# Optimization experiments

Hardware: AMD Instinct MI355X
Metric: run time of the kernel (lower is better)

Reference implementation:

```python
import jax, jax.numpy as jnp
import numpy as np

D_K = 64  # per-head dim, used as softmax scale (matches __init__ d_k)

def setup_inputs() -> dict:
    key = jax.random.key(0)
    kq, kk, kv, km = jax.random.split(key, 4)
    B, H, S, D = 2, 16, 2048, D_K
    q = jax.random.normal(kq, (B, H, S, D), dtype=jnp.float32)
    k = jax.random.normal(kk, (B, H, S, D), dtype=jnp.float32)
    v = jax.random.normal(kv, (B, H, S, D), dtype=jnp.float32)
    mask = jax.random.randint(km, (B, 1, S, S), 0, 2).astype(jnp.bool_)
    return {"q": q, "k": k, "v": v, "mask": mask}

def reference(q, k, v, mask):
    # attn = (q / sqrt(d_k)) @ k^T  -> [B,H,S,S]
    scale = 1.0 / jnp.sqrt(jnp.float32(D_K))
    attn = jnp.einsum("bhqd,bhkd->bhqk", q * scale, k)
    # faithful to torch masked_fill(mask, -1e-09) -- note tiny value, not -1e9
    attn = jnp.where(mask, jnp.float32(-1e-9), attn)
    weights = jax.nn.softmax(attn, axis=-1)  # dropout p=0.0 -> identity
    output = jnp.einsum("bhqk,bhkd->bhqd", weights, v)
    return (output, weights)
```

## Files before the change

### kernel.cpp

```cpp
#include <hip/hip_runtime.h>
#include <hip/hip_bf16.h>


namespace {

constexpr int kS = 2048;
constexpr int kD = 64;
constexpr int kBH = 32;
constexpr int kTQW = 16;
constexpr int kNW = 4;
constexpr int kTQB = kTQW * kNW;
constexpr int kChunk = 64;
constexpr int kNC = kS / kChunk;
constexpr int kNB = kBH * (kS / kTQB);
constexpr size_t kWOff = (size_t)kBH * kS * kD;

typedef __attribute__((ext_vector_type(8))) short bf16x8;
typedef __attribute__((ext_vector_type(4))) short bf16x4;
typedef __attribute__((ext_vector_type(4))) float f32x4;

__device__ inline short f2bf(float f) {
  union { float f; unsigned u; } x; x.f = f;
  return (short)((x.u + 0x7fffu + ((x.u >> 16) & 1u)) >> 16);
}

__device__ inline unsigned pk2bf(float a, float b) {
  return (unsigned)(unsigned short)f2bf(a) | ((unsigned)(unsigned short)f2bf(b) << 16);
}

__device__ inline bf16x8 cvt8(float4 a, float4 b, float scale) {
  bf16x8 f;
  f[0] = f2bf(a.x * scale); f[1] = f2bf(a.y * scale);
  f[2] = f2bf(a.z * scale); f[3] = f2bf(a.w * scale);
  f[4] = f2bf(b.x * scale); f[5] = f2bf(b.y * scale);
  f[6] = f2bf(b.z * scale); f[7] = f2bf(b.w * scale);
  return f;
}

__device__ inline f32x4 mfma32(bf16x8 a, bf16x8 b, f32x4 c) {
  return __builtin_amdgcn_mfma_f32_16x16x32_bf16(a, b, c, 0, 0, 0);
}

__device__ inline f32x4 mfma16(bf16x4 a, bf16x4 b, f32x4 c) {
#if __has_builtin(__builtin_amdgcn_mfma_f32_16x16x16bf16_1k)
  return __builtin_amdgcn_mfma_f32_16x16x16bf16_1k(a, b, c, 0, 0, 0);
#elif __has_builtin(__builtin_amdgcn_mfma_f32_16x16x16_bf16)
  return __builtin_amdgcn_mfma_f32_16x16x16_bf16(a, b, c, 0, 0, 0);
#else
  f32x4 d = c;
  asm volatile("v_mfma_f32_16x16x16_bf16 %0, %1, %2, %0" : "+v"(d) : "v"(a), "v"(b));
  return d;
#endif
}

__device__ inline void block_sync_lds() {
  asm volatile("s_waitcnt lgkmcnt(0)" ::: "memory");
  __builtin_amdgcn_s_barrier();
  asm volatile("" ::: "memory");
}

__global__ __launch_bounds__(256, 4) void attn_fused(
    const float* __restrict__ qg, const float* __restrict__ kg,
    const float* __restrict__ vg, const unsigned int* __restrict__ mg,
    float* __restrict__ outg) {
  __shared__ __align__(16) short SH[18432];
  short (*K0)[72] = (short(*)[72])(SH);
  short (*K1)[72] = (short(*)[72])(SH + 4608);
  short (*V0)[72] = (short(*)[72])(SH + 9216);
  short (*V1)[72] = (short(*)[72])(SH + 13824);

  const int tid  = threadIdx.x;
  const int wv   = tid >> 6;
  const int lane = tid & 63;
  const int l15  = lane & 15;
  const int quad = lane >> 4;

  const int bid  = blockIdx.x;
  const int work = ((bid & 7) << 7) | (bid >> 3);
  const int qt   = work & 31;
  const int bh   = work >> 5;
  const int b    = bh >> 4;
  const int q0b  = qt * kTQB;

  int allW32 = 1, allI32 = 1, allBF = 1;
#pragma unroll
  for (int i = 0; i < 64; ++i) {
    const unsigned u = mg[i];
    const unsigned lo = u & 0xFFFFu, hi = u >> 16;
    allW32 &= (int)(u == 0u || u == 0x3F800000u);
    allI32 &= (int)(u == 0u || u == 1u);
    allBF  &= (int)((lo == 0u || lo == 0x3F80u) && (hi == 0u || hi == 0x3F80u));
  }
  int msz;
  if (allI32)      msz = 4;
  else if (allW32) msz = 4;
  else if (allBF)  msz = 2;
  else             msz = 1;
  const unsigned char* mB = (const unsigned char*)mg + (size_t)b * kS * kS * msz;

  const float* qbase = qg + (size_t)bh * kS * kD;
  const float* kbase = kg + (size_t)bh * kS * kD;
  const float* vbase = vg + (size_t)bh * kS * kD;
  float* obase = outg + (size_t)bh * kS * kD;
  float* wbase = outg + kWOff + (size_t)bh * kS * kS;

  const int qrow = q0b + wv * kTQW + l15;

  bf16x8 aq[2];
#pragma unroll
  for (int dh = 0; dh < 2; ++dh) {
    const float* p = qbase + (size_t)qrow * kD + dh * 32 + quad * 8;
    aq[dh] = cvt8(*(const float4*)p, *(const float4*)(p + 4), 0.125f);
  }

  const int si = tid >> 2;
  const int sj = (tid & 3) << 4;
  const int vd = (tid & 7) << 3;
  const int vk = (tid >> 3) << 1;
  float4 rk[4], rv[4];

  auto k_issue = [&](int c) {
    const float* p = kbase + (size_t)(c * kChunk + si) * kD + sj;
    rk[0] = *(const float4*)p;       rk[1] = *(const float4*)(p + 4);
    rk[2] = *(const float4*)(p + 8); rk[3] = *(const float4*)(p + 12);
  };
  auto k_write = [&](short (*Kdst)[72]) {
    *(bf16x8*)&Kdst[si][sj]     = cvt8(rk[0], rk[1], 1.0f);
    *(bf16x8*)&Kdst[si][sj + 8] = cvt8(rk[2], rk[3], 1.0f);
  };

  auto v_issue = [&](int c) {
    const float* p = vbase + (size_t)(c * kChunk + vk) * kD + vd;
    rv[0] = *(const float4*)p;        rv[1] = *(const float4*)(p + 4);
    rv[2] = *(const float4*)(p + kD); rv[3] = *(const float4*)(p + kD + 4);
  };
  auto v_write = [&](short (*Vdst)[72]) {
    const float* lo = (const float*)&rv[0];
    const float* hi = (const float*)&rv[2];
#pragma unroll
    for (int d = 0; d < 8; ++d) {
      const int dd = vd + d;
      const int ps = (vk >> 1) ^ (((dd >> 3) & 7) << 2);
      *(unsigned*)&Vdst[dd][2 * ps] = pk2bf(lo[d], hi[d]);
    }
  };

  uint4 mr[4];
  unsigned mu[4];
  auto m_issue = [&](int c) {
    const int col0 = c * kChunk + quad * 4;
#pragma unroll
    for (int t = 0; t < 4; ++t) {
      const size_t e = (size_t)qrow * kS + col0 + t * 16;
      if (msz == 1)      mr[t].x = *(const unsigned*)(mB + e);
      else if (msz == 4) mr[t]   = *(const uint4*)((const unsigned*)mB + e);
      else {
        const unsigned* p = (const unsigned*)((const unsigned short*)mB + e);
        mr[t].x = p[0]; mr[t].y = p[1];
      }
    }
  };
  auto m_conv = [&]() {
#pragma unroll
    for (int t = 0; t < 4; ++t) {
      if (msz == 1)      mu[t] = mr[t].x;
      else if (msz == 4) mu[t] = (mr[t].x ? 1u : 0u) | ((mr[t].y ? 1u : 0u) << 8) |
                                 ((mr[t].z ? 1u : 0u) << 16) | ((mr[t].w ? 1u : 0u) << 24);
      else {
        const unsigned a = mr[t].x, bb = mr[t].y;
        mu[t] = ((a & 0xFFFFu) ? 1u : 0u) | (((a >> 16) ? 1u : 0u) << 8) |
                (((bb & 0xFFFFu) ? 1u : 0u) << 16) | (((bb >> 16) ? 1u : 0u) << 24);
      }
    }
  };

  float lsum = 0.f;
  k_issue(0); k_write(K0); k_issue(1);
  block_sync_lds();
  for (int c = 0; c < kNC; ++c) {
    m_issue(c);
    if (c + 1 < kNC) k_write((c & 1) ? K0 : K1);
    if (c + 2 < kNC) k_issue(c + 2);
    m_conv();
    short (*K)[72] = (c & 1) ? K1 : K0;
#pragma unroll
    for (int t = 0; t < 4; ++t) {
      bf16x8 f0 = *(const bf16x8*)&K[t * 16 + l15][quad * 8];
      bf16x8 f1 = *(const bf16x8*)&K[t * 16 + l15][32 + quad * 8];
      f32x4 acc = {0.f, 0.f, 0.f, 0.f};
      acc = mfma32(f0, aq[0], acc);
      acc = mfma32(f1, aq[1], acc);
#pragma unroll
      for (int r = 0; r < 4; ++r) {
        const float e = __expf(acc[r]);
        lsum += ((mu[t] >> (8 * r)) & 0xFFu) ? 1.0f : e;
      }
    }
    block_sync_lds();
  }

  lsum += __shfl_xor(lsum, 16);
  lsum += __shfl_xor(lsum, 32);
  const float inv = 1.0f / lsum;

  f32x4 acco[4];
#pragma unroll
  for (int d = 0; d < 4; ++d) acco[d] = (f32x4){0.f, 0.f, 0.f, 0.f};

  k_issue(0); v_issue(0);
  k_write(K0); v_write(V0);
  k_issue(1); v_issue(1);
  block_sync_lds();
  float* const wrow = wbase + (size_t)qrow * kS;
  for (int c = 0; c < kNC; ++c) {
    m_issue(c);
    if (c + 1 < kNC) { k_write((c & 1) ? K0 : K1); v_write((c & 1) ? V0 : V1); }
    if (c + 2 < kNC) { k_issue(c + 2); v_issue(c + 2); }
    m_conv();
    short (*K)[72] = (c & 1) ? K1 : K0;
    short (*V)[72] = (c & 1) ? V1 : V0;
    __builtin_amdgcn_s_setprio(1);
#pragma unroll
    for (int t = 0; t < 4; ++t) {
      bf16x8 f0 = *(const bf16x8*)&K[t * 16 + l15][quad * 8];
      bf16x8 f1 = *(const bf16x8*)&K[t * 16 + l15][32 + quad * 8];
      f32x4 acc = {0.f, 0.f, 0.f, 0.f};
      acc = mfma32(f0, aq[0], acc);
      acc = mfma32(f1, aq[1], acc);
      const unsigned m = mu[t];
      const float w0 = ((m       & 0xFFu) ? 1.0f : __expf(acc[0])) * inv;
      const float w1 = ((m >> 8  & 0xFFu) ? 1.0f : __expf(acc[1])) * inv;
      const float w2 = ((m >> 16 & 0xFFu) ? 1.0f : __expf(acc[2])) * inv;
      const float w3 = ((m >> 24        ) ? 1.0f : __expf(acc[3])) * inv;
      *(f32x4*)(wrow + c * kChunk + t * 16 + quad * 4) = (f32x4){w0, w1, w2, w3};
      const bf16x4 wfrag = {f2bf(w0), f2bf(w1), f2bf(w2), f2bf(w3)};
#pragma unroll
      for (int dt = 0; dt < 4; ++dt) {
        const int dd = dt * 16 + l15;
        const int pp = (8 * t + 2 * quad) ^ (((dd >> 3) & 7) << 2);
        const bf16x4 vfrag = *(const bf16x4*)&V[dd][2 * pp];
        acco[dt] = mfma16(vfrag, wfrag, acco[dt]);
      }
    }
    __builtin_amdgcn_s_setprio(0);
    block_sync_lds();
  }

#pragma unroll
  for (int dt = 0; dt < 4; ++dt)
    *(f32x4*)(obase + (size_t)qrow * kD + dt * 16 + quad * 4) = acco[dt];
}

}

extern "C" void kernel_launch(void* const* d_in, const int* in_sizes, int n_in,
                              void* d_out, int out_size, void* d_ws, size_t ws_size,
                              hipStream_t stream) {
  const float* q = (const float*)d_in[0];
  const float* k = (const float*)d_in[1];
  const float* v = (const float*)d_in[2];
  const unsigned int* mask = (const unsigned int*)d_in[3];
  float* out = (float*)d_out;
  attn_fused<<<dim3(kNB), dim3(256), 0, stream>>>(q, k, v, mask, out);
}
```

Measured before the change: 905.1 us.

## Stage mask tiles through LDS as bitmasks with coalesced prefetched loads

Mask loading moves from per-lane scattered global reads, issued and consumed within the same chunk, to coalesced cooperative loads of the block's 64x64 mask tile. Each tile is compressed to a 16-bit-per-thread bitmask and double-buffered in LDS two chunks ahead, like K/V. Lanes then read one 64-bit word from LDS per chunk. This removes exposed mask-load latency and uncoalesced access, at the cost of a little extra LDS and bit-packing ALU work. The first pass also gains s_setprio around its MFMA section.

Result: faster. 811.5 us (-10.3%).

```diff
diff --git a/kernel.cpp b/kernel.cpp
--- a/kernel.cpp
+++ b/kernel.cpp
@@ -63,11 +63,13 @@
     const float* __restrict__ qg, const float* __restrict__ kg,
     const float* __restrict__ vg, const unsigned int* __restrict__ mg,
     float* __restrict__ outg) {
-  __shared__ __align__(16) short SH[18432];
+  __shared__ __align__(16) short SH[18944];
   short (*K0)[72] = (short(*)[72])(SH);
   short (*K1)[72] = (short(*)[72])(SH + 4608);
   short (*V0)[72] = (short(*)[72])(SH + 9216);
   short (*V1)[72] = (short(*)[72])(SH + 13824);
+  unsigned short* Msk0 = (unsigned short*)(SH + 18432);
+  unsigned short* Msk1 = (unsigned short*)(SH + 18688);
 
   const int tid  = threadIdx.x;
   const int wv   = tid >> 6;
@@ -105,6 +107,7 @@
   float* wbase = outg + kWOff + (size_t)bh * kS * kS;
 
   const int qrow = q0b + wv * kTQW + l15;
+  const int mrow = wv * kTQW + l15;
 
   bf16x8 aq[2];
 #pragma unroll
@@ -113,11 +116,13 @@
     aq[dh] = cvt8(*(const float4*)p, *(const float4*)(p + 4), 0.125f);
   }
 
-  const int si = tid >> 2;
-  const int sj = (tid & 3) << 4;
-  const int vd = (tid & 7) << 3;
-  const int vk = (tid >> 3) << 1;
+  const int si  = tid >> 2;
+  const int sj  = (tid & 3) << 4;
+  const int sjw = tid & 3;
+  const int vd  = (tid & 7) << 3;
+  const int vk  = (tid >> 3) << 1;
   float4 rk[4], rv[4];
+  uint4 mrg[4];
 
   auto k_issue = [&](int c) {
     const float* p = kbase + (size_t)(c * kChunk + si) * kD + sj;
@@ -145,44 +150,67 @@
     }
   };
 
-  uint4 mr[4];
-  unsigned mu[4];
   auto m_issue = [&](int c) {
-    const int col0 = c * kChunk + quad * 4;
-#pragma unroll
-    for (int t = 0; t < 4; ++t) {
-      const size_t e = (size_t)qrow * kS + col0 + t * 16;
-      if (msz == 1)      mr[t].x = *(const unsigned*)(mB + e);
-      else if (msz == 4) mr[t]   = *(const uint4*)((const unsigned*)mB + e);
-      else {
-        const unsigned* p = (const unsigned*)((const unsigned short*)mB + e);
-        mr[t].x = p[0]; mr[t].y = p[1];
-      }
-    }
-  };
-  auto m_conv = [&]() {
-#pragma unroll
-    for (int t = 0; t < 4; ++t) {
-      if (msz == 1)      mu[t] = mr[t].x;
-      else if (msz == 4) mu[t] = (mr[t].x ? 1u : 0u) | ((mr[t].y ? 1u : 0u) << 8) |
-                                 ((mr[t].z ? 1u : 0u) << 16) | ((mr[t].w ? 1u : 0u) << 24);
-      else {
-        const unsigned a = mr[t].x, bb = mr[t].y;
-        mu[t] = ((a & 0xFFFFu) ? 1u : 0u) | (((a >> 16) ? 1u : 0u) << 8) |
-                (((bb & 0xFFFFu) ? 1u : 0u) << 16) | (((bb >> 16) ? 1u : 0u) << 24);
-      }
-    }
+    const size_t base = (size_t)(q0b + si) * kS + (size_t)(c * kChunk) + sjw * 16;
+    if (msz == 4) {
+      const uint4* p = (const uint4*)((const unsigned*)mB + base);
+      mrg[0] = p[0]; mrg[1] = p[1]; mrg[2] = p[2]; mrg[3] = p[3];
+    } else if (msz == 2) {
+      const uint4* p = (const uint4*)((const unsigned short*)mB + base);
+      mrg[0] = p[0]; mrg[1] = p[1];
+    } else {
+      mrg[0] = *(const uint4*)(mB + base);
+    }
+  };
+  auto m_write = [&](unsigned short* Mdst) {
+    unsigned bits = 0;
+    if (msz == 4) {
+#pragma unroll
+      for (int g = 0; g < 4; ++g) {
+        const uint4 e = mrg[g];
+        bits |= (e.x ? 1u : 0u) << (4 * g + 0);
+        bits |= (e.y ? 1u : 0u) << (4 * g + 1);
+        bits |= (e.z ? 1u : 0u) << (4 * g + 2);
+        bits |= (e.w ? 1u : 0u) << (4 * g + 3);
+      }
+    } else if (msz == 2) {
+#pragma unroll
+      for (int g = 0; g < 2; ++g) {
+        const uint4 e = mrg[g];
+        bits |= ((e.x & 0xFFFFu) ? 1u : 0u) << (8 * g + 0);
+        bits |= ((e.x >> 16)     ? 1u : 0u) << (8 * g + 1);
+        bits |= ((e.y & 0xFFFFu) ? 1u : 0u) << (8 * g + 2);
+        bits |= ((e.y >> 16)     ? 1u : 0u) << (8 * g + 3);
+        bits |= ((e.z & 0xFFFFu) ? 1u : 0u) << (8 * g + 4);
+        bits |= ((e.z >> 16)     ? 1u : 0u) << (8 * g + 5);
+        bits |= ((e.w & 0xFFFFu) ? 1u : 0u) << (8 * g + 6);
+        bits |= ((e.w >> 16)     ? 1u : 0u) << (8 * g + 7);
+      }
+    } else {
+      const uint4 e = mrg[0];
+#pragma unroll
+      for (int by = 0; by < 4; ++by) {
+        bits |= (((e.x >> (8 * by)) & 0xFFu) ? 1u : 0u) << (0 + by);
+        bits |= (((e.y >> (8 * by)) & 0xFFu) ? 1u : 0u) << (4 + by);
+        bits |= (((e.z >> (8 * by)) & 0xFFu) ? 1u : 0u) << (8 + by);
+        bits |= (((e.w >> (8 * by)) & 0xFFu) ? 1u : 0u) << (12 + by);
+      }
+    }
+    Mdst[si * 4 + sjw] = (unsigned short)bits;
   };
 
   float lsum = 0.f;
-  k_issue(0); k_write(K0); k_issue(1);
+  k_issue(0); m_issue(0);
+  k_write(K0); m_write(Msk0);
+  k_issue(1); m_issue(1);
   block_sync_lds();
   for (int c = 0; c < kNC; ++c) {
-    m_issue(c);
-    if (c + 1 < kNC) k_write((c & 1) ? K0 : K1);
-    if (c + 2 < kNC) k_issue(c + 2);
-    m_conv();
+    if (c + 1 < kNC) { k_write((c & 1) ? K0 : K1); m_write((c & 1) ? Msk0 : Msk1); }
+    if (c + 2 < kNC) { k_issue(c + 2); m_issue(c + 2); }
     short (*K)[72] = (c & 1) ? K1 : K0;
+    const unsigned short* M = (c & 1) ? Msk1 : Msk0;
+    const unsigned long long mbits = *(const unsigned long long*)&M[mrow * 4];
+    __builtin_amdgcn_s_setprio(1);
 #pragma unroll
     for (int t = 0; t < 4; ++t) {
       bf16x8 f0 = *(const bf16x8*)&K[t * 16 + l15][quad * 8];
@@ -190,12 +218,14 @@
       f32x4 acc = {0.f, 0.f, 0.f, 0.f};
       acc = mfma32(f0, aq[0], acc);
       acc = mfma32(f1, aq[1], acc);
+      const unsigned nib = (unsigned)(mbits >> (16 * t + 4 * quad)) & 0xFu;
 #pragma unroll
       for (int r = 0; r < 4; ++r) {
         const float e = __expf(acc[r]);
-        lsum += ((mu[t] >> (8 * r)) & 0xFFu) ? 1.0f : e;
-      }
-    }
+        lsum += (nib & (1u << r)) ? 1.0f : e;
+      }
+    }
+    __builtin_amdgcn_s_setprio(0);
     block_sync_lds();
   }
 
@@ -207,18 +237,21 @@
 #pragma unroll
   for (int d = 0; d < 4; ++d) acco[d] = (f32x4){0.f, 0.f, 0.f, 0.f};
 
-  k_issue(0); v_issue(0);
-  k_write(K0); v_write(V0);
-  k_issue(1); v_issue(1);
+  k_issue(0); v_issue(0); m_issue(0);
+  k_write(K0); v_write(V0); m_write(Msk0);
+  k_issue(1); v_issue(1); m_issue(1);
   block_sync_lds();
   float* const wrow = wbase + (size_t)qrow * kS;
   for (int c = 0; c < kNC; ++c) {
-    m_issue(c);
-    if (c + 1 < kNC) { k_write((c & 1) ? K0 : K1); v_write((c & 1) ? V0 : V1); }
-    if (c + 2 < kNC) { k_issue(c + 2); v_issue(c + 2); }
-    m_conv();
+    if (c + 1 < kNC) {
+      k_write((c & 1) ? K0 : K1); v_write((c & 1) ? V0 : V1);
+      m_write((c & 1) ? Msk0 : Msk1);
+    }
+    if (c + 2 < kNC) { k_issue(c + 2); v_issue(c + 2); m_issue(c + 2); }
     short (*K)[72] = (c & 1) ? K1 : K0;
     short (*V)[72] = (c & 1) ? V1 : V0;
+    const unsigned short* M = (c & 1) ? Msk1 : Msk0;
+    const unsigned long long mbits = *(const unsigned long long*)&M[mrow * 4];
     __builtin_amdgcn_s_setprio(1);
 #pragma unroll
     for (int t = 0; t < 4; ++t) {
@@ -227,11 +260,11 @@
       f32x4 acc = {0.f, 0.f, 0.f, 0.f};
       acc = mfma32(f0, aq[0], acc);
       acc = mfma32(f1, aq[1], acc);
-      const unsigned m = mu[t];
-      const float w0 = ((m       & 0xFFu) ? 1.0f : __expf(acc[0])) * inv;
-      const float w1 = ((m >> 8  & 0xFFu) ? 1.0f : __expf(acc[1])) * inv;
-      const float w2 = ((m >> 16 & 0xFFu) ? 1.0f : __expf(acc[2])) * inv;
-      const float w3 = ((m >> 24        ) ? 1.0f : __expf(acc[3])) * inv;
+      const unsigned nib = (unsigned)(mbits >> (16 * t + 4 * quad)) & 0xFu;
+      const float w0 = ((nib & 1u) ? 1.0f : __expf(acc[0])) * inv;
+      const float w1 = ((nib & 2u) ? 1.0f : __expf(acc[1])) * inv;
+      const float w2 = ((nib & 4u) ? 1.0f : __expf(acc[2])) * inv;
+      const float w3 = ((nib & 8u) ? 1.0f : __expf(acc[3])) * inv;
       *(f32x4*)(wrow + c * kChunk + t * 16 + quad * 4) = (f32x4){w0, w1, w2, w3};
       const bf16x4 wfrag = {f2bf(w0), f2bf(w1), f2bf(w2), f2bf(w3)};
 #pragma unroll
```
